# Kernel tuning notes

Measured on AMD Instinct MI355X. Metric: run time of the kernel, lower is better.

## Reference

```python
import jax, jax.numpy as jnp
import numpy as np

N_BRANCH, N_LAYER = 4, 3
B, T, D_IN = 4, 1024, 32
D_MODEL, D_INNER, D_STATE, D_CONV, DT_RANK = 128, 256, 16, 4, 8
EMBED = 64
MAX_NORM = 10.0  # safe_expmap0 tangent-norm clip
EPS = 1e-7


def setup_inputs() -> dict:
    key = jax.random.key(0)
    ks = jax.random.split(key, 12)
    def nrm(k, shp, s=0.02):
        return s * jax.random.normal(k, shp, dtype=jnp.float32)
    A_init = jnp.log(jnp.arange(1, D_STATE + 1, dtype=jnp.float32))
    return {
        "trend": jax.random.normal(ks[0], (B, T, D_IN), jnp.float32),
        "seasonal_coarse": jax.random.normal(ks[1], (B, T, D_IN), jnp.float32),
        "seasonal_fine": jax.random.normal(ks[2], (B, T, D_IN), jnp.float32),
        "residual": jax.random.normal(ks[3], (B, T, D_IN), jnp.float32),
        "W_ip": nrm(ks[4], (N_BRANCH, D_IN, D_MODEL)),
        "b_ip": jnp.zeros((N_BRANCH, D_MODEL), jnp.float32),
        "W_in": nrm(ks[5], (N_BRANCH, N_LAYER, D_MODEL, 2 * D_INNER)),
        "conv_w": nrm(ks[6], (N_BRANCH, N_LAYER, D_INNER, D_CONV), 0.1),
        "conv_b": jnp.zeros((N_BRANCH, N_LAYER, D_INNER), jnp.float32),
        "W_x": nrm(ks[7], (N_BRANCH, N_LAYER, D_INNER, DT_RANK + 2 * D_STATE)),
        "W_dt": nrm(ks[8], (N_BRANCH, N_LAYER, DT_RANK, D_INNER), 0.1),
        "b_dt": jnp.full((N_BRANCH, N_LAYER, D_INNER), -4.6, jnp.float32),  # softplus ~ 0.01
        "A_log": jnp.broadcast_to(A_init, (N_BRANCH, N_LAYER, D_INNER, D_STATE)),
        "D_param": jnp.ones((N_BRANCH, N_LAYER, D_INNER), jnp.float32),
        "W_out": nrm(ks[9], (N_BRANCH, N_LAYER, D_INNER, D_MODEL)),
        "W_op": nrm(ks[10], (N_BRANCH, D_MODEL, EMBED)),
        "b_op": jnp.zeros((N_BRANCH, EMBED), jnp.float32),
        "eff_scale": jnp.asarray(0.1, jnp.float32),
    }


def _mamba_layer(x, Win, cw, cb, Wx, Wdt, bdt, Alog, Dp, Wout):
    # x: [B, T, d_model]
    Tlen = x.shape[1]
    xz = x @ Win                                   # [B,T,2*di]
    xp, z = jnp.split(xz, 2, axis=-1)
    # causal depthwise conv1d, kernel D_CONV
    xpad = jnp.pad(xp, ((0, 0), (D_CONV - 1, 0), (0, 0)))
    xc = sum(xpad[:, k:k + Tlen, :] * cw[:, k] for k in range(D_CONV))
    xc = jax.nn.silu(xc + cb)                      # [B,T,di]
    dbl = xc @ Wx                                  # [B,T,r+2s]
    dt = jax.nn.softplus(dbl[..., :DT_RANK] @ Wdt + bdt)   # [B,T,di]
    Bm = dbl[..., DT_RANK:DT_RANK + D_STATE]       # [B,T,s]
    Cm = dbl[..., DT_RANK + D_STATE:]              # [B,T,s]
    A = -jnp.exp(Alog)                             # [di,s]
    dA = jnp.exp(dt[..., None] * A)                # [B,T,di,s]
    dBx = (dt * xc)[..., None] * Bm[:, :, None, :] # [B,T,di,s]

    def step(h, inp):
        dA_t, dBx_t, C_t = inp
        h = dA_t * h + dBx_t
        return h, jnp.einsum('bds,bs->bd', h, C_t)

    h0 = jnp.zeros((x.shape[0], D_INNER, D_STATE), x.dtype)
    _, ys = jax.lax.scan(step, h0, (jnp.swapaxes(dA, 0, 1),
                                     jnp.swapaxes(dBx, 0, 1),
                                     jnp.swapaxes(Cm, 0, 1)))
    y = jnp.swapaxes(ys, 0, 1) + Dp * xc
    return (y * jax.nn.silu(z)) @ Wout


def _embed(x, Wip, bip, Wins, cws, cbs, Wxs, Wdts, bdts, Alogs, Dps, Wouts, Wop, bop):
    h = x @ Wip + bip
    for l in range(N_LAYER):
        h = _mamba_layer(h, Wins[l], cws[l], cbs[l], Wxs[l], Wdts[l], bdts[l],
                         Alogs[l], Dps[l], Wouts[l])
    return h.mean(axis=1) @ Wop + bop              # [B, EMBED]


def _expmap0(v):
    # safe expmap0 on Lorentz (k=1): clip tangent norm at MAX_NORM
    n = jnp.linalg.norm(v, axis=-1, keepdims=True)
    nc = jnp.clip(n, EPS, MAX_NORM)
    v = v * (nc / jnp.maximum(n, EPS))
    return jnp.concatenate([jnp.cosh(nc), jnp.sinh(nc) / nc * v], axis=-1)


def _projx(x):
    sp = x[..., 1:]
    t = jnp.sqrt(1.0 + jnp.sum(sp * sp, axis=-1, keepdims=True))
    return jnp.concatenate([t, sp], axis=-1)


def _logmap0(x):
    sp = x[..., 1:]
    t = jnp.maximum(x[..., :1], 1.0 + EPS)
    d = jnp.arccosh(t)
    spn = jnp.maximum(jnp.linalg.norm(sp, axis=-1, keepdims=True), EPS)
    return d * sp / spn


def _forward(trend, seasonal_coarse, seasonal_fine, residual,
             W_ip, b_ip, W_in, conv_w, conv_b, W_x, W_dt, b_dt,
             A_log, D_param, W_out, W_op, b_op, eff_scale):
    xs = [trend, seasonal_coarse, seasonal_fine, residual]
    z_t = [
        _embed(xs[b], W_ip[b], b_ip[b], W_in[b], conv_w[b], conv_b[b], W_x[b],
               W_dt[b], b_dt[b], A_log[b], D_param[b], W_out[b], W_op[b], b_op[b])
        for b in range(N_BRANCH)
    ]
    es = jnp.tanh(eff_scale)
    z_h = [_projx(_expmap0(z * es)) for z in z_t]
    us = [_logmap0(zh) for zh in z_h]
    combined_tangent = us[0] + us[1] + us[2] + us[3]
    combined_h = _projx(_expmap0(combined_tangent * es))
    return (*z_t, *z_h, combined_tangent, combined_h)


def reference(trend, seasonal_coarse, seasonal_fine, residual,
              W_ip, b_ip, W_in, conv_w, conv_b, W_x, W_dt, b_dt,
              A_log, D_param, W_out, W_op, b_op, eff_scale):
    return _forward(trend, seasonal_coarse, seasonal_fine, residual,
                    W_ip, b_ip, W_in, conv_w, conv_b, W_x, W_dt, b_dt,
                    A_log, D_param, W_out, W_op, b_op, eff_scale)
```

## Files before the change

### kernel.cpp

```cpp
#include <hip/hip_runtime.h>
#include <math.h>

#define NBR 4
#define NLAY 3
#define Bk 4
#define Tk 1024
#define DIN 32
#define DMODEL 128
#define DINNER 256
#define DSTATE 16
#define DTRANK 8
#define EMBEDk 64
#define BT (Bk*Tk)
#define EPSF 1e-7f
#define MAXNF 10.0f
#define LCH 64
#define NCH (Tk/LCH)
#define UF 8
#define NWB 320

typedef __bf16 bf16x8 __attribute__((ext_vector_type(8)));
typedef float  f32x4  __attribute__((ext_vector_type(4)));
typedef unsigned short u16x8 __attribute__((ext_vector_type(8)));

__device__ __forceinline__ float siluf(float x){ return x / (1.f + __expf(-x)); }
__device__ __forceinline__ float softplusf(float x){ return (x > 20.f) ? x : log1pf(__expf(x)); }
__device__ __forceinline__ unsigned short f2b(float x){
    union { float f; unsigned u; } v; v.f = x;
    unsigned r = v.u + 0x7FFF + ((v.u >> 16) & 1);
    return (unsigned short)(r >> 16);
}
__device__ __forceinline__ float b2f(unsigned short u){
    union { unsigned u; float f; } v; v.u = ((unsigned)u) << 16; return v.f;
}

__device__ __forceinline__ void dA_pow(float q, float* dA){
    dA[0] = q;             dA[1] = q * q;
    dA[2] = dA[1] * dA[0]; dA[3] = dA[1] * dA[1];
    dA[4] = dA[3] * dA[0]; dA[5] = dA[3] * dA[1];
    dA[6] = dA[3] * dA[2]; dA[7] = dA[3] * dA[3];
    #pragma unroll
    for (int s = 8; s < 16; ++s) dA[s] = dA[s - 8] * dA[7];
}
__device__ __forceinline__ void dA_exp(float dtv, const float* Aa, float* dA){
    #pragma unroll
    for (int s = 0; s < 16; ++s) dA[s] = __expf(dtv * Aa[s]);
}

template<int MODE>
__global__ __launch_bounds__(256) void bgemm_k(
    const unsigned short* __restrict__ Ab, long aBr, int K,
    const unsigned short* __restrict__ Bt, long bBr,
    float* __restrict__ C0, long c0Br,
    float* __restrict__ C1, long c1Br,
    unsigned short* __restrict__ Cb, long cbBr,
    const float* __restrict__ bias, long biasBr)
{
    const int br = blockIdx.z;
    Ab += (long)br * aBr;
    Bt += (long)br * bBr;
    if (MODE == 1 || MODE == 3) C0 += (long)br * c0Br;
    if (MODE == 0 || MODE == 3) C1 += (long)br * c1Br;
    if (MODE == 0) Cb += (long)br * cbBr;
    if (MODE == 3) bias += (long)br * biasBr;
    const int m0 = blockIdx.x * 64, n0 = blockIdx.y * 64;
    __shared__ __align__(16) unsigned short As[8 * 64 * 8];
    __shared__ __align__(16) unsigned short Bs[8 * 64 * 8];
    const int tid = threadIdx.x;
    const int lane = tid & 63, w = tid >> 6;
    const int wm = w >> 1, wn = w & 1;
    const int quad = lane >> 4, l15 = lane & 15;
    f32x4 acc00 = {0,0,0,0}, acc01 = {0,0,0,0}, acc10 = {0,0,0,0}, acc11 = {0,0,0,0};
    for (int kc = 0; kc < K; kc += 64) {
        #pragma unroll
        for (int it = 0; it < 2; ++it) {
            const int c = tid + it * 256;
            const int r = c & 63, kch = c >> 6;
            *(u16x8*)&As[(kch * 64 + r) * 8] =
                *(const u16x8*)(Ab + (long)(m0 + r) * K + kc + kch * 8);
            *(u16x8*)&Bs[(kch * 64 + r) * 8] =
                *(const u16x8*)(Bt + (long)(n0 + r) * K + kc + kch * 8);
        }
        __syncthreads();
        #pragma unroll
        for (int k0 = 0; k0 < 64; k0 += 32) {
            const int kch = (k0 >> 3) + quad;
            bf16x8 a0 = *(const bf16x8*)&As[(kch * 64 + wm * 32 +      l15) * 8];
            bf16x8 a1 = *(const bf16x8*)&As[(kch * 64 + wm * 32 + 16 + l15) * 8];
            bf16x8 b0 = *(const bf16x8*)&Bs[(kch * 64 + wn * 32 +      l15) * 8];
            bf16x8 b1 = *(const bf16x8*)&Bs[(kch * 64 + wn * 32 + 16 + l15) * 8];
            acc00 = __builtin_amdgcn_mfma_f32_16x16x32_bf16(a0, b0, acc00, 0, 0, 0);
            acc01 = __builtin_amdgcn_mfma_f32_16x16x32_bf16(a0, b1, acc01, 0, 0, 0);
            acc10 = __builtin_amdgcn_mfma_f32_16x16x32_bf16(a1, b0, acc10, 0, 0, 0);
            acc11 = __builtin_amdgcn_mfma_f32_16x16x32_bf16(a1, b1, acc11, 0, 0, 0);
        }
        __syncthreads();
    }
    #pragma unroll
    for (int e = 0; e < 4; ++e) {
        f32x4 a = (e == 0) ? acc00 : (e == 1) ? acc01 : (e == 2) ? acc10 : acc11;
        const int msub = (e >> 1) * 16, nsub = (e & 1) * 16;
        const int col = n0 + wn * 32 + nsub + l15;
        #pragma unroll
        for (int r = 0; r < 4; ++r) {
            const int row = m0 + wm * 32 + msub + quad * 4 + r;
            const float v = a[r];
            if (MODE == 0) {
                if (n0 < 256) Cb[(long)row * 256 + col] = f2b(v);
                else          C1[(long)row * 256 + (col - 256)] = siluf(v);
            } else if (MODE == 1) {
                C0[(long)row * 128 + col] = v;
            } else {
                if (col < 256)      C0[(long)row * 256 + col] = softplusf(v + bias[col]);
                else if (col < 288) C1[(long)row * 32 + (col - 256)] = v;
            }
        }
    }
}

__global__ __launch_bounds__(256) void prepT_k(
    const float* __restrict__ W, unsigned short* __restrict__ o,
    int Kd, int Nd, long wBr, long oBr)
{
    const int br = blockIdx.z;
    W += (long)br * wBr; o += (long)br * oBr;
    const int n0 = blockIdx.x * 64, k0 = blockIdx.y * 64;
    __shared__ float tile[64][65];
    const int t = threadIdx.x;
    #pragma unroll
    for (int i = 0; i < 16; ++i) {
        int idx = t + i * 256;
        int kl = idx >> 6, nl = idx & 63;
        tile[kl][nl] = W[(long)(k0 + kl) * Nd + n0 + nl];
    }
    __syncthreads();
    #pragma unroll
    for (int i = 0; i < 16; ++i) {
        int idx = t + i * 256;
        int nl = idx >> 6, kl = idx & 63;
        o[(long)(n0 + nl) * Kd + k0 + kl] = f2b(tile[kl][nl]);
    }
}

__global__ __launch_bounds__(256) void sgemmW_k(
    const float* __restrict__ Wout, const float* __restrict__ Win,
    float* __restrict__ Wtmp)
{
    const int z = blockIdx.z, p = z >> 2, br = z & 3;
    const float* A  = Wout + (long)(br * NLAY + p) * DINNER * DMODEL;
    const float* Bw = Win  + (long)(br * NLAY + p + 1) * DMODEL * 512;
    float* C = Wtmp + (long)z * DINNER * 512;
    const int m0 = blockIdx.x * 64, n0 = blockIdx.y * 64;
    __shared__ float As[32][68];
    __shared__ float Bs[32][68];
    const int tid = threadIdx.x;
    const int tx = tid & 15, ty = tid >> 4;
    float acc[4][4] = {};
    for (int kc = 0; kc < DMODEL; kc += 32) {
        #pragma unroll
        for (int it = 0; it < 2; ++it) {
            int id = tid + it * 256;
            int r = id >> 3, c4 = (id & 7) << 2;
            float4 v = *(const float4*)(A + (long)(m0 + r) * DMODEL + kc + c4);
            As[c4+0][r] = v.x; As[c4+1][r] = v.y; As[c4+2][r] = v.z; As[c4+3][r] = v.w;
            int rb = id >> 4, cb = (id & 15) << 2;
            *(float4*)&Bs[rb][cb] = *(const float4*)(Bw + (long)(kc + rb) * 512 + n0 + cb);
        }
        __syncthreads();
        #pragma unroll
        for (int kk = 0; kk < 32; ++kk) {
            float4 a4 = *(const float4*)&As[kk][ty << 2];
            float4 b4 = *(const float4*)&Bs[kk][tx << 2];
            float av[4] = {a4.x, a4.y, a4.z, a4.w};
            float bv[4] = {b4.x, b4.y, b4.z, b4.w};
            #pragma unroll
            for (int i = 0; i < 4; ++i)
                #pragma unroll
                for (int j = 0; j < 4; ++j)
                    acc[i][j] = fmaf(av[i], bv[j], acc[i][j]);
        }
        __syncthreads();
    }
    #pragma unroll
    for (int i = 0; i < 4; ++i) {
        int row = m0 + (ty << 2) + i, col = n0 + (tx << 2);
        float4 v4; v4.x = acc[i][0]; v4.y = acc[i][1]; v4.z = acc[i][2]; v4.w = acc[i][3];
        *(float4*)(C + (long)row * 512 + col) = v4;
    }
}

__global__ __launch_bounds__(256) void prepC_k(
    const float* __restrict__ Wx, const float* __restrict__ Wdt,
    unsigned short* __restrict__ o)
{
    const int n = blockIdx.x, bl = blockIdx.y;
    const int k = threadIdx.x;
    const float* WxP = Wx + (long)bl * DINNER * 40;
    float v;
    if (n < 256) {
        const float* WdtP = Wdt + (long)bl * DTRANK * DINNER;
        float s = 0.f;
        #pragma unroll
        for (int r = 0; r < 8; ++r) s = fmaf(WxP[k * 40 + r], WdtP[r * DINNER + n], s);
        v = s;
    } else if (n < 288) {
        v = WxP[k * 40 + 8 + (n - 256)];
    } else {
        v = 0.f;
    }
    o[(long)bl * NWB * DINNER + (long)n * DINNER + k] = f2b(v);
}

__global__ __launch_bounds__(256) void proj_k(
    const float* __restrict__ A0, const float* __restrict__ A1,
    const float* __restrict__ A2, const float* __restrict__ A3,
    const float* __restrict__ Bw, const float* __restrict__ bias,
    unsigned short* __restrict__ Cb)
{
    const int br = blockIdx.z;
    const float* A = (br == 1) ? A1 : (br == 2) ? A2 : (br == 3) ? A3 : A0;
    Bw   += (long)br * DIN * DMODEL;
    bias += (long)br * DMODEL;
    Cb   += (long)br * BT * DMODEL;
    const int m0 = blockIdx.x * 64, n0 = blockIdx.y * 64;
    __shared__ float As[32][68];
    __shared__ float Bs[32][68];
    const int tid = threadIdx.x;
    const int tx = tid & 15, ty = tid >> 4;
    float acc[4][4] = {};
    {
        #pragma unroll
        for (int it = 0; it < 2; ++it) {
            int id = tid + it * 256;
            int r = id >> 3, c4 = (id & 7) << 2;
            float4 v = *(const float4*)(A + (long)(m0 + r) * DIN + c4);
            As[c4+0][r] = v.x; As[c4+1][r] = v.y; As[c4+2][r] = v.z; As[c4+3][r] = v.w;
            int rb = id >> 4, cb = (id & 15) << 2;
            *(float4*)&Bs[rb][cb] = *(const float4*)(Bw + (long)rb * DMODEL + n0 + cb);
        }
        __syncthreads();
        #pragma unroll
        for (int kk = 0; kk < 32; ++kk) {
            float4 a4 = *(const float4*)&As[kk][ty << 2];
            float4 b4 = *(const float4*)&Bs[kk][tx << 2];
            float av[4] = {a4.x, a4.y, a4.z, a4.w};
            float bv[4] = {b4.x, b4.y, b4.z, b4.w};
            #pragma unroll
            for (int i = 0; i < 4; ++i)
                #pragma unroll
                for (int j = 0; j < 4; ++j)
                    acc[i][j] = fmaf(av[i], bv[j], acc[i][j]);
        }
    }
    const int col = n0 + (tx << 2);
    float bs[4];
    #pragma unroll
    for (int j = 0; j < 4; ++j) bs[j] = bias[col + j];
    #pragma unroll
    for (int i = 0; i < 4; ++i) {
        const int row = m0 + (ty << 2) + i;
        #pragma unroll
        for (int j = 0; j < 4; ++j)
            Cb[(long)row * DMODEL + col + j] = f2b(acc[i][j] + bs[j]);
    }
}

__global__ __launch_bounds__(256) void conv_k(
    const unsigned short* __restrict__ xp, const float* __restrict__ cw,
    const float* __restrict__ cb, unsigned short* __restrict__ xcb, int layer)
{
    const int br = blockIdx.y;
    const long base = (long)br * BT * DINNER;
    const int idx = blockIdx.x * 256 + threadIdx.x;
    const int d = idx & (DINNER - 1);
    const int row = idx >> 8;
    const int t = row & (Tk - 1);
    const float4 w4 = *(const float4*)(cw + ((long)(br * NLAY + layer) * DINNER + d) * 4);
    const float wv[4] = {w4.x, w4.y, w4.z, w4.w};
    float acc = cb[(br * NLAY + layer) * DINNER + d];
    const unsigned short* xpb = xp + base + idx;
    #pragma unroll
    for (int k = 0; k < 4; ++k) {
        int tt = t + k - 3;
        if (tt >= 0) acc = fmaf(b2f(xpb[(long)(k - 3) * DINNER]), wv[k], acc);
    }
    xcb[base + idx] = f2b(siluf(acc));
}

__global__ __launch_bounds__(256) void scan1_k(
    const float* __restrict__ dtb, const unsigned short* __restrict__ xcb,
    const float* __restrict__ bcb, const float* __restrict__ Alog,
    float* __restrict__ recbuf, int layer)
{
    const int c = blockIdx.x, b = blockIdx.y, br = blockIdx.z;
    const int d = threadIdx.x;
    const float* Ap = Alog + ((long)(br * NLAY + layer) * DINNER + d) * DSTATE;
    float Aa[16];
    bool pw = true;
    #pragma unroll
    for (int s = 0; s < 16; ++s) {
        Aa[s] = -__expf(Ap[s]);
        pw = pw && (fabsf(Aa[s] + (float)(s + 1)) < 1e-3f);
    }
    const long rbase = (long)br * BT + (long)b * Tk + (long)c * LCH;
    const float* dtp = dtb + rbase * DINNER + d;
    const unsigned short* xcp = xcb + rbase * DINNER + d;
    __shared__ float bcs[LCH * 32];
    {
        const float4* g = (const float4*)(bcb + rbase * 32);
        float4* l = (float4*)bcs;
        l[d] = g[d]; l[d + 256] = g[d + 256];
    }
    float dtc[UF], xcc[UF];
    #pragma unroll
    for (int u = 0; u < UF; ++u) {
        dtc[u] = dtp[(long)u * DINNER];
        xcc[u] = b2f(xcp[(long)u * DINNER]);
    }
    __syncthreads();
    float h[16];
    #pragma unroll
    for (int s = 0; s < 16; ++s) h[s] = 0.f;
    float sumdt = 0.f;
    for (int base = 0; base < LCH; base += UF) {
        const int nb = (base + UF < LCH) ? base + UF : base;
        float dtn[UF], xcn[UF];
        #pragma unroll
        for (int u = 0; u < UF; ++u) {
            dtn[u] = dtp[(long)(nb + u) * DINNER];
            xcn[u] = b2f(xcp[(long)(nb + u) * DINNER]);
        }
        #pragma unroll
        for (int u = 0; u < UF; ++u) {
            const int t = base + u;
            const float dtv = dtc[u];
            const float dtxc = dtv * xcc[u];
            sumdt += dtv;
            float dA[16];
            if (pw) dA_pow(__expf(-dtv), dA);
            else    dA_exp(dtv, Aa, dA);
            const float* bcT = bcs + t * 32;
            #pragma unroll
            for (int s = 0; s < 16; ++s)
                h[s] = fmaf(dA[s], h[s], dtxc * bcT[s]);
        }
        #pragma unroll
        for (int u = 0; u < UF; ++u) { dtc[u] = dtn[u]; xcc[u] = xcn[u]; }
    }
    float* sb = recbuf + (((long)(br * 4 + b) * (NCH - 1) + c) * 17) * 256 + d;
    #pragma unroll
    for (int s = 0; s < 16; ++s) sb[s * 256] = h[s];
    sb[16 * 256] = sumdt;
}

__global__ __launch_bounds__(256) void scan3_k(
    const float* __restrict__ dtb, const unsigned short* __restrict__ xcb,
    const float* __restrict__ bcb, const float* __restrict__ zb,
    const float* __restrict__ Alog, const float* __restrict__ Dpar,
    const float* __restrict__ recbuf, unsigned short* __restrict__ yzb, int layer)
{
    const int c = blockIdx.x, b = blockIdx.y, br = blockIdx.z;
    const int d = threadIdx.x;
    const float* Ap = Alog + ((long)(br * NLAY + layer) * DINNER + d) * DSTATE;
    float Aa[16];
    bool pw = true;
    #pragma unroll
    for (int s = 0; s < 16; ++s) {
        Aa[s] = -__expf(Ap[s]);
        pw = pw && (fabsf(Aa[s] + (float)(s + 1)) < 1e-3f);
    }
    float h[16];
    #pragma unroll
    for (int s = 0; s < 16; ++s) h[s] = 0.f;
    if (c > 0) {
        const float* recB = recbuf + ((long)(br * 4 + b) * (NCH - 1)) * 17 * 256 + d;
        float rh[16], rs;
        #pragma unroll
        for (int s = 0; s < 16; ++s) rh[s] = recB[s * 256];
        rs = recB[16 * 256];
        for (int cc = 0; cc < c; ++cc) {
            float nh[16], ns = 0.f;
            if (cc + 1 < c) {
                const float* r2 = recB + (long)(cc + 1) * 17 * 256;
                #pragma unroll
                for (int s = 0; s < 16; ++s) nh[s] = r2[s * 256];
                ns = r2[16 * 256];
            } else {
                #pragma unroll
                for (int s = 0; s < 16; ++s) nh[s] = 0.f;
            }
            float P[16];
            if (pw) dA_pow(__expf(-rs), P);
            else    dA_exp(rs, Aa, P);
            #pragma unroll
            for (int s = 0; s < 16; ++s) h[s] = fmaf(h[s], P[s], rh[s]);
            #pragma unroll
            for (int s = 0; s < 16; ++s) rh[s] = nh[s];
            rs = ns;
        }
    }
    const float Dp = Dpar[(br * NLAY + layer) * DINNER + d];
    const long rbase = (long)br * BT + (long)b * Tk + (long)c * LCH;
    const float* dtp = dtb + rbase * DINNER + d;
    const unsigned short* xcp = xcb + rbase * DINNER + d;
    const float* zp  = zb  + rbase * DINNER + d;
    unsigned short* yp = yzb + rbase * DINNER + d;
    __shared__ float bcs[LCH * 32];
    {
        const float4* g = (const float4*)(bcb + rbase * 32);
        float4* l = (float4*)bcs;
        l[d] = g[d]; l[d + 256] = g[d + 256];
    }
    float dtc[UF], xcc[UF], zc[UF];
    #pragma unroll
    for (int u = 0; u < UF; ++u) {
        dtc[u] = dtp[(long)u * DINNER];
        xcc[u] = b2f(xcp[(long)u * DINNER]);
        zc[u]  = zp[(long)u * DINNER];
    }
    __syncthreads();
    for (int base = 0; base < LCH; base += UF) {
        const int nb = (base + UF < LCH) ? base + UF : base;
        float dtn[UF], xcn[UF], zn[UF];
        #pragma unroll
        for (int u = 0; u < UF; ++u) {
            dtn[u] = dtp[(long)(nb + u) * DINNER];
            xcn[u] = b2f(xcp[(long)(nb + u) * DINNER]);
            zn[u]  = zp[(long)(nb + u) * DINNER];
        }
        #pragma unroll
        for (int u = 0; u < UF; ++u) {
            const int t = base + u;
            const float dtv = dtc[u], xcv = xcc[u];
            const float dtxc = dtv * xcv;
            float dA[16];
            if (pw) dA_pow(__expf(-dtv), dA);
            else    dA_exp(dtv, Aa, dA);
            const float* bcT = bcs + t * 32;
            #pragma unroll
            for (int s = 0; s < 16; ++s)
                h[s] = fmaf(dA[s], h[s], dtxc * bcT[s]);
            float y0 = 0.f, y1 = 0.f, y2 = 0.f, y3 = 0.f;
            #pragma unroll
            for (int s = 0; s < 16; s += 4) {
                y0 = fmaf(h[s+0], bcT[16+s+0], y0);
                y1 = fmaf(h[s+1], bcT[16+s+1], y1);
                y2 = fmaf(h[s+2], bcT[16+s+2], y2);
                y3 = fmaf(h[s+3], bcT[16+s+3], y3);
            }
            const float y = (y0 + y1) + (y2 + y3) + Dp * xcv;
            yp[(long)t * DINNER] = f2b(y * zc[u]);
        }
        #pragma unroll
        for (int u = 0; u < UF; ++u) { dtc[u] = dtn[u]; xcc[u] = xcn[u]; zc[u] = zn[u]; }
    }
}

__global__ __launch_bounds__(128) void meanop_k(
    const float* __restrict__ hbuf, const float* __restrict__ Wop,
    const float* __restrict__ bop, float* __restrict__ outzt)
{
    const int br = blockIdx.x >> 2, b = blockIdx.x & 3;
    const int tid = threadIdx.x;
    const float* hp = hbuf + ((long)br * BT + (long)b * Tk) * DMODEL + tid;
    float s = 0.f;
    for (int t = 0; t < Tk; ++t) s += hp[(long)t * DMODEL];
    __shared__ float hm[DMODEL];
    hm[tid] = s * (1.0f / Tk);
    __syncthreads();
    if (tid < EMBEDk) {
        float acc = bop[br * EMBEDk + tid];
        for (int k = 0; k < DMODEL; ++k)
            acc = fmaf(hm[k], Wop[(long)br * DMODEL * EMBEDk + k * EMBEDk + tid], acc);
        outzt[br * (Bk * EMBEDk) + b * EMBEDk + tid] = acc;
    }
}

__global__ __launch_bounds__(64) void final_k(
    const float* __restrict__ zt, float* __restrict__ out, const float* __restrict__ eff)
{
    const float es = tanhf(eff[0]);
    __shared__ float us[NBR][Bk][EMBEDk];
    const int t = threadIdx.x;
    if (t < 16) {
        const int br = t >> 2, b = t & 3;
        const float* z = zt + br * (Bk * EMBEDk) + b * EMBEDk;
        float n2 = 0.f;
        for (int e = 0; e < EMBEDk; ++e) { float v = z[e] * es; n2 = fmaf(v, v, n2); }
        const float n  = sqrtf(n2);
        const float nc = fminf(fmaxf(n, EPSF), MAXNF);
        const float sc = nc / fmaxf(n, EPSF);
        const float sh = sinhf(nc) / nc;
        const float fac = es * sc * sh;
        float* zh = out + 1024 + br * (Bk * (EMBEDk + 1)) + b * (EMBEDk + 1);
        float sp2 = 0.f;
        for (int e = 0; e < EMBEDk; ++e) {
            float spv = z[e] * fac;
            sp2 = fmaf(spv, spv, sp2);
            zh[1 + e] = spv;
            us[br][b][e] = spv;
        }
        const float t0 = sqrtf(1.f + sp2);
        zh[0] = t0;
        const float dd  = acoshf(fmaxf(t0, 1.f + EPSF));
        const float spn = fmaxf(sqrtf(sp2), EPSF);
        const float rr  = dd / spn;
        for (int e = 0; e < EMBEDk; ++e) us[br][b][e] *= rr;
    }
    __syncthreads();
    if (t < 4) {
        const int b = t;
        float ct[EMBEDk];
        float* cto = out + 2064 + b * EMBEDk;
        for (int e = 0; e < EMBEDk; ++e) {
            float v = us[0][b][e] + us[1][b][e] + us[2][b][e] + us[3][b][e];
            ct[e] = v; cto[e] = v;
        }
        float n2 = 0.f;
        for (int e = 0; e < EMBEDk; ++e) { float v = ct[e] * es; n2 = fmaf(v, v, n2); }
        const float n  = sqrtf(n2);
        const float nc = fminf(fmaxf(n, EPSF), MAXNF);
        const float sc = nc / fmaxf(n, EPSF);
        const float sh = sinhf(nc) / nc;
        const float fac = es * sc * sh;
        float* ch = out + 2320 + b * (EMBEDk + 1);
        float sp2 = 0.f;
        for (int e = 0; e < EMBEDk; ++e) {
            float spv = ct[e] * fac;
            sp2 = fmaf(spv, spv, sp2);
            ch[1 + e] = spv;
        }
        ch[0] = sqrtf(1.f + sp2);
    }
}

extern "C" void kernel_launch(void* const* d_in, const int* in_sizes, int n_in,
                              void* d_out, int out_size, void* d_ws, size_t ws_size,
                              hipStream_t stream)
{
    const float* X0 = (const float*)d_in[0];
    const float* X1 = (const float*)d_in[1];
    const float* X2 = (const float*)d_in[2];
    const float* X3 = (const float*)d_in[3];
    const float* W_ip   = (const float*)d_in[4];
    const float* b_ip   = (const float*)d_in[5];
    const float* W_in   = (const float*)d_in[6];
    const float* conv_w = (const float*)d_in[7];
    const float* conv_b = (const float*)d_in[8];
    const float* W_x    = (const float*)d_in[9];
    const float* W_dt   = (const float*)d_in[10];
    const float* b_dt   = (const float*)d_in[11];
    const float* A_log  = (const float*)d_in[12];
    const float* D_par  = (const float*)d_in[13];
    const float* W_out  = (const float*)d_in[14];
    const float* W_op   = (const float*)d_in[15];
    const float* b_op   = (const float*)d_in[16];
    const float* eff    = (const float*)d_in[17];
    float* out = (float*)d_out;
    float* ws  = (float*)d_ws;

    float* buf_z  = ws;
    float* buf_dt = buf_z  + (long)NBR * BT * DINNER;
    float* buf_bc = buf_dt + (long)NBR * BT * DINNER;
    float* buf_h  = buf_bc + (long)NBR * BT * 32;
    float* recbuf = buf_h  + (long)NBR * BT * DMODEL;
    float* Wtmp   = recbuf + (long)16 * (NCH - 1) * 17 * 256;
    unsigned short* h_bf  = (unsigned short*)(Wtmp + (long)8 * DINNER * 512);
    unsigned short* xp_bf = h_bf  + (long)NBR * BT * DMODEL;
    unsigned short* xc_bf = xp_bf + (long)NBR * BT * DINNER;
    unsigned short* yz_bf = xc_bf + (long)NBR * BT * DINNER;
    unsigned short* Win0T = yz_bf + (long)NBR * BT * DINNER;
    unsigned short* WfT   = Win0T + (long)NBR * 512 * DMODEL;
    unsigned short* WcT   = WfT   + (long)8 * 512 * DINNER;
    unsigned short* Wo2T  = WcT   + (long)NBR * NLAY * NWB * DINNER;

    prepT_k<<<dim3(8, 2, NBR), 256, 0, stream>>>(
        W_in, Win0T, DMODEL, 512, (long)NLAY * DMODEL * 512, (long)512 * DMODEL);
    sgemmW_k<<<dim3(4, 8, 8), 256, 0, stream>>>(W_out, W_in, Wtmp);
    prepT_k<<<dim3(8, 4, 8), 256, 0, stream>>>(
        Wtmp, WfT, DINNER, 512, (long)DINNER * 512, (long)512 * DINNER);
    prepC_k<<<dim3(NWB, NBR * NLAY), 256, 0, stream>>>(W_x, W_dt, WcT);
    prepT_k<<<dim3(2, 4, NBR), 256, 0, stream>>>(
        W_out + (long)2 * DINNER * DMODEL, Wo2T, DINNER, DMODEL,
        (long)NLAY * DINNER * DMODEL, (long)DMODEL * DINNER);

    proj_k<<<dim3(BT / 64, DMODEL / 64, NBR), 256, 0, stream>>>(
        X0, X1, X2, X3, W_ip, b_ip, h_bf);

    for (int l = 0; l < NLAY; ++l) {
        if (l == 0) {
            bgemm_k<0><<<dim3(BT / 64, 8, NBR), 256, 0, stream>>>(
                h_bf, (long)BT * DMODEL, DMODEL,
                Win0T, (long)512 * DMODEL,
                nullptr, 0, buf_z, (long)BT * DINNER,
                xp_bf, (long)BT * DINNER, nullptr, 0);
        } else {
            bgemm_k<0><<<dim3(BT / 64, 8, NBR), 256, 0, stream>>>(
                yz_bf, (long)BT * DINNER, DINNER,
                WfT + (long)(l - 1) * 4 * 512 * DINNER, (long)512 * DINNER,
                nullptr, 0, buf_z, (long)BT * DINNER,
                xp_bf, (long)BT * DINNER, nullptr, 0);
        }
        conv_k<<<dim3((BT * DINNER) / 256, NBR), 256, 0, stream>>>(
            xp_bf, conv_w, conv_b, xc_bf, l);
        bgemm_k<3><<<dim3(BT / 64, NWB / 64, NBR), 256, 0, stream>>>(
            xc_bf, (long)BT * DINNER, DINNER,
            WcT + (long)l * NWB * DINNER, (long)NLAY * NWB * DINNER,
            buf_dt, (long)BT * DINNER, buf_bc, (long)BT * 32,
            nullptr, 0, b_dt + l * DINNER, (long)NLAY * DINNER);
        scan1_k<<<dim3(NCH - 1, Bk, NBR), 256, 0, stream>>>(
            buf_dt, xc_bf, buf_bc, A_log, recbuf, l);
        scan3_k<<<dim3(NCH, Bk, NBR), 256, 0, stream>>>(
            buf_dt, xc_bf, buf_bc, buf_z, A_log, D_par, recbuf, yz_bf, l);
        if (l == NLAY - 1) {
            bgemm_k<1><<<dim3(BT / 64, DMODEL / 64, NBR), 256, 0, stream>>>(
                yz_bf, (long)BT * DINNER, DINNER,
                Wo2T, (long)DMODEL * DINNER,
                buf_h, (long)BT * DMODEL, nullptr, 0,
                nullptr, 0, nullptr, 0);
        }
    }

    meanop_k<<<16, 128, 0, stream>>>(buf_h, W_op, b_op, out);
    final_k<<<1, 64, 0, stream>>>(out, out, eff);
}
```

Before: 469.0 us.

## Reorder time-mean before final out-projection, vectorize conv, use direct LDS loads in GEMM

Because mean over time is linear, the final W_out GEMM over all tokens is replaced by a time-sum of yz followed by a small matvec through W_out and W_op. This drops a full GEMM, its weight transpose prep and the fp32 h buffer. The depthwise conv now handles 8 channels per thread with 16-byte loads and stores, and the GEMM tile loads use global_load_lds to write straight into shared memory. The mean is now summed from bf16-rounded yz rather than an fp32 GEMM output, so rounding order shifts slightly.

Measured after the change: 425.1 us. 1.1x faster.

```diff
diff --git a/kernel.cpp b/kernel.cpp
--- a/kernel.cpp
+++ b/kernel.cpp
@@ -34,6 +34,13 @@
     union { unsigned u; float f; } v; v.u = ((unsigned)u) << 16; return v.f;
 }
 
+__device__ __forceinline__ void gll16(const void* g, void* l){
+    __builtin_amdgcn_global_load_lds(
+        (const __attribute__((address_space(1))) unsigned int*)g,
+        (__attribute__((address_space(3))) unsigned int*)l,
+        16, 0, 0);
+}
+
 __device__ __forceinline__ void dA_pow(float q, float* dA){
     dA[0] = q;             dA[1] = q * q;
     dA[2] = dA[1] * dA[0]; dA[3] = dA[1] * dA[1];
@@ -59,7 +66,7 @@
     const int br = blockIdx.z;
     Ab += (long)br * aBr;
     Bt += (long)br * bBr;
-    if (MODE == 1 || MODE == 3) C0 += (long)br * c0Br;
+    if (MODE == 3) C0 += (long)br * c0Br;
     if (MODE == 0 || MODE == 3) C1 += (long)br * c1Br;
     if (MODE == 0) Cb += (long)br * cbBr;
     if (MODE == 3) bias += (long)br * biasBr;
@@ -74,12 +81,9 @@
     for (int kc = 0; kc < K; kc += 64) {
         #pragma unroll
         for (int it = 0; it < 2; ++it) {
-            const int c = tid + it * 256;
-            const int r = c & 63, kch = c >> 6;
-            *(u16x8*)&As[(kch * 64 + r) * 8] =
-                *(const u16x8*)(Ab + (long)(m0 + r) * K + kc + kch * 8);
-            *(u16x8*)&Bs[(kch * 64 + r) * 8] =
-                *(const u16x8*)(Bt + (long)(n0 + r) * K + kc + kch * 8);
+            const int kch = w + it * 4;
+            gll16(Ab + (long)(m0 + lane) * K + kc + kch * 8, &As[(kch * 64) * 8]);
+            gll16(Bt + (long)(n0 + lane) * K + kc + kch * 8, &Bs[(kch * 64) * 8]);
         }
         __syncthreads();
         #pragma unroll
@@ -108,8 +112,6 @@
             if (MODE == 0) {
                 if (n0 < 256) Cb[(long)row * 256 + col] = f2b(v);
                 else          C1[(long)row * 256 + (col - 256)] = siluf(v);
-            } else if (MODE == 1) {
-                C0[(long)row * 128 + col] = v;
             } else {
                 if (col < 256)      C0[(long)row * 256 + col] = softplusf(v + bias[col]);
                 else if (col < 288) C1[(long)row * 32 + (col - 256)] = v;
@@ -271,20 +273,33 @@
 {
     const int br = blockIdx.y;
     const long base = (long)br * BT * DINNER;
-    const int idx = blockIdx.x * 256 + threadIdx.x;
-    const int d = idx & (DINNER - 1);
-    const int row = idx >> 8;
-    const int t = row & (Tk - 1);
-    const float4 w4 = *(const float4*)(cw + ((long)(br * NLAY + layer) * DINNER + d) * 4);
-    const float wv[4] = {w4.x, w4.y, w4.z, w4.w};
-    float acc = cb[(br * NLAY + layer) * DINNER + d];
-    const unsigned short* xpb = xp + base + idx;
+    const long idx8 = ((long)blockIdx.x * 256 + threadIdx.x) * 8;
+    const int d0 = (int)(idx8 & (DINNER - 1));
+    const long row = idx8 >> 8;
+    const int t = (int)(row & (Tk - 1));
+    const float* cwp = cw + ((long)(br * NLAY + layer) * DINNER + d0) * 4;
+    const float* cbp = cb + (long)(br * NLAY + layer) * DINNER + d0;
+    u16x8 in[4];
     #pragma unroll
     for (int k = 0; k < 4; ++k) {
-        int tt = t + k - 3;
-        if (tt >= 0) acc = fmaf(b2f(xpb[(long)(k - 3) * DINNER]), wv[k], acc);
-    }
-    xcb[base + idx] = f2b(siluf(acc));
+        const int tt = t + k - 3;
+        if (tt >= 0) {
+            in[k] = *(const u16x8*)(xp + base + idx8 + (long)(k - 3) * DINNER);
+        } else {
+            #pragma unroll
+            for (int j = 0; j < 8; ++j) in[k][j] = 0;
+        }
+    }
+    u16x8 o;
+    #pragma unroll
+    for (int j = 0; j < 8; ++j) {
+        float acc = cbp[j];
+        #pragma unroll
+        for (int k = 0; k < 4; ++k)
+            acc = fmaf(b2f(in[k][j]), cwp[j * 4 + k], acc);
+        o[j] = f2b(siluf(acc));
+    }
+    *(u16x8*)(xcb + base + idx8) = o;
 }
 
 __global__ __launch_bounds__(256) void scan1_k(
@@ -456,23 +471,59 @@
     }
 }
 
-__global__ __launch_bounds__(128) void meanop_k(
-    const float* __restrict__ hbuf, const float* __restrict__ Wop,
-    const float* __restrict__ bop, float* __restrict__ outzt)
-{
-    const int br = blockIdx.x >> 2, b = blockIdx.x & 3;
+__global__ __launch_bounds__(256) void csum1_k(
+    const unsigned short* __restrict__ yz, float* __restrict__ part)
+{
+    const int ch = blockIdx.x, brb = blockIdx.y;
+    const int br = brb >> 2, b = brb & 3;
+    const long rbase = (long)br * BT + (long)b * Tk + (long)ch * 128;
     const int tid = threadIdx.x;
-    const float* hp = hbuf + ((long)br * BT + (long)b * Tk) * DMODEL + tid;
+    const int cg = tid & 31;
+    const int ro = tid >> 5;
+    const unsigned short* p = yz + (rbase + ro) * DINNER + cg * 8;
+    float acc[8] = {0,0,0,0,0,0,0,0};
+    for (int it = 0; it < 16; ++it) {
+        u16x8 v = *(const u16x8*)(p + (long)it * 8 * DINNER);
+        #pragma unroll
+        for (int j = 0; j < 8; ++j) acc[j] += b2f(v[j]);
+    }
+    __shared__ float sm[8][256];
+    #pragma unroll
+    for (int j = 0; j < 8; ++j) sm[ro][cg * 8 + j] = acc[j];
+    __syncthreads();
     float s = 0.f;
-    for (int t = 0; t < Tk; ++t) s += hp[(long)t * DMODEL];
-    __shared__ float hm[DMODEL];
-    hm[tid] = s * (1.0f / Tk);
+    #pragma unroll
+    for (int r = 0; r < 8; ++r) s += sm[r][tid];
+    part[((long)brb * 8 + ch) * 256 + tid] = s;
+}
+
+__global__ __launch_bounds__(256) void csum2_k(
+    const float* __restrict__ part, const float* __restrict__ Wout,
+    const float* __restrict__ Wop, const float* __restrict__ bop,
+    float* __restrict__ outzt)
+{
+    const int brb = blockIdx.x;
+    const int br = brb >> 2, b = brb & 3;
+    const int tid = threadIdx.x;
+    __shared__ float v[256];
+    __shared__ float u[128];
+    float s = 0.f;
+    #pragma unroll
+    for (int ch = 0; ch < 8; ++ch) s += part[((long)brb * 8 + ch) * 256 + tid];
+    v[tid] = s * (1.0f / Tk);
+    __syncthreads();
+    if (tid < 128) {
+        const float* W2 = Wout + (long)(br * NLAY + 2) * DINNER * DMODEL;
+        float a = 0.f;
+        for (int k = 0; k < 256; ++k) a = fmaf(v[k], W2[k * DMODEL + tid], a);
+        u[tid] = a;
+    }
     __syncthreads();
     if (tid < EMBEDk) {
-        float acc = bop[br * EMBEDk + tid];
-        for (int k = 0; k < DMODEL; ++k)
-            acc = fmaf(hm[k], Wop[(long)br * DMODEL * EMBEDk + k * EMBEDk + tid], acc);
-        outzt[br * (Bk * EMBEDk) + b * EMBEDk + tid] = acc;
+        float a = bop[br * EMBEDk + tid];
+        for (int k = 0; k < 128; ++k)
+            a = fmaf(u[k], Wop[(long)br * DMODEL * EMBEDk + k * EMBEDk + tid], a);
+        outzt[br * (Bk * EMBEDk) + b * EMBEDk + tid] = a;
     }
 }
 
@@ -562,8 +613,8 @@
     float* buf_z  = ws;
     float* buf_dt = buf_z  + (long)NBR * BT * DINNER;
     float* buf_bc = buf_dt + (long)NBR * BT * DINNER;
-    float* buf_h  = buf_bc + (long)NBR * BT * 32;
-    float* recbuf = buf_h  + (long)NBR * BT * DMODEL;
+    float* part   = buf_bc + (long)NBR * BT * 32;
+    float* recbuf = part   + (long)NBR * BT * DMODEL;
     float* Wtmp   = recbuf + (long)16 * (NCH - 1) * 17 * 256;
     unsigned short* h_bf  = (unsigned short*)(Wtmp + (long)8 * DINNER * 512);
     unsigned short* xp_bf = h_bf  + (long)NBR * BT * DMODEL;
@@ -572,7 +623,6 @@
     unsigned short* Win0T = yz_bf + (long)NBR * BT * DINNER;
     unsigned short* WfT   = Win0T + (long)NBR * 512 * DMODEL;
     unsigned short* WcT   = WfT   + (long)8 * 512 * DINNER;
-    unsigned short* Wo2T  = WcT   + (long)NBR * NLAY * NWB * DINNER;
 
     prepT_k<<<dim3(8, 2, NBR), 256, 0, stream>>>(
         W_in, Win0T, DMODEL, 512, (long)NLAY * DMODEL * 512, (long)512 * DMODEL);
@@ -580,9 +630,6 @@
     prepT_k<<<dim3(8, 4, 8), 256, 0, stream>>>(
         Wtmp, WfT, DINNER, 512, (long)DINNER * 512, (long)512 * DINNER);
     prepC_k<<<dim3(NWB, NBR * NLAY), 256, 0, stream>>>(W_x, W_dt, WcT);
-    prepT_k<<<dim3(2, 4, NBR), 256, 0, stream>>>(
-        W_out + (long)2 * DINNER * DMODEL, Wo2T, DINNER, DMODEL,
-        (long)NLAY * DINNER * DMODEL, (long)DMODEL * DINNER);
 
     proj_k<<<dim3(BT / 64, DMODEL / 64, NBR), 256, 0, stream>>>(
         X0, X1, X2, X3, W_ip, b_ip, h_bf);
@@ -601,7 +648,7 @@
                 nullptr, 0, buf_z, (long)BT * DINNER,
                 xp_bf, (long)BT * DINNER, nullptr, 0);
         }
-        conv_k<<<dim3((BT * DINNER) / 256, NBR), 256, 0, stream>>>(
+        conv_k<<<dim3((BT * DINNER) / (256 * 8), NBR), 256, 0, stream>>>(
             xp_bf, conv_w, conv_b, xc_bf, l);
         bgemm_k<3><<<dim3(BT / 64, NWB / 64, NBR), 256, 0, stream>>>(
             xc_bf, (long)BT * DINNER, DINNER,
@@ -612,15 +659,9 @@
             buf_dt, xc_bf, buf_bc, A_log, recbuf, l);
         scan3_k<<<dim3(NCH, Bk, NBR), 256, 0, stream>>>(
             buf_dt, xc_bf, buf_bc, buf_z, A_log, D_par, recbuf, yz_bf, l);
-        if (l == NLAY - 1) {
-            bgemm_k<1><<<dim3(BT / 64, DMODEL / 64, NBR), 256, 0, stream>>>(
-                yz_bf, (long)BT * DINNER, DINNER,
-                Wo2T, (long)DMODEL * DINNER,
-                buf_h, (long)BT * DMODEL, nullptr, 0,
-                nullptr, 0, nullptr, 0);
-        }
-    }
-
-    meanop_k<<<16, 128, 0, stream>>>(buf_h, W_op, b_op, out);
+    }
+
+    csum1_k<<<dim3(8, 16), 256, 0, stream>>>(yz_bf, part);
+    csum2_k<<<16, 256, 0, stream>>>(part, W_out, W_op, b_op, out);
     final_k<<<1, 64, 0, stream>>>(out, out, eff);
 }
```
